# Kernel tuning notes

Measured on AMD Instinct MI355X. Metric: run time of the kernel, lower is better.

Reference implementation:

```python
import jax, jax.numpy as jnp
import numpy as np

HYP_C = 0.1
TAU = 0.1
MRG = 0.1
CLIP_R = 2.3
BS = 1024
NB_PROXIES = 256
SZ_EMBED = 128
T_BATCH = BS * 50
T_LCA = NB_PROXIES * 50


@jax.custom_vjp
def artanh(x):
    xc = jnp.clip(x, -1.0 + 1e-5, 1.0 - 1e-5)
    return 0.5 * (jnp.log1p(xc) - jnp.log1p(-xc))

def _artanh_fwd(x):
    xc = jnp.clip(x, -1.0 + 1e-5, 1.0 - 1e-5)
    return 0.5 * (jnp.log1p(xc) - jnp.log1p(-xc)), xc

def _artanh_bwd(xc, g):
    return (g / (1.0 - xc * xc),)

artanh.defvjp(_artanh_fwd, _artanh_bwd)


@jax.custom_vjp
def riemannian_fix(x):
    # identity fwd; bwd rescales euclidean grad to riemannian grad on the ball
    return x

def _riem_fwd(x):
    return x, x

def _riem_bwd(x, g):
    scale = ((1.0 - HYP_C * jnp.sum(x * x, axis=-1, keepdims=True)) ** 2) / 4.0
    return (g * scale,)

riemannian_fix.defvjp(_riem_fwd, _riem_bwd)


def expmap0(x, c):
    sqrt_c = c ** 0.5
    xn = jnp.maximum(jnp.linalg.norm(x, axis=-1, keepdims=True), 1e-5)
    return jnp.tanh(sqrt_c * xn) * x / (sqrt_c * xn)


def project(x, c):
    norm = jnp.maximum(jnp.linalg.norm(x, axis=-1, keepdims=True), 1e-5)
    maxnorm = (1.0 - 1e-3) / (c ** 0.5)
    return jnp.where(norm > maxnorm, x / norm * maxnorm, x)


def to_poincare(x, c, clip_r):
    xn = jnp.linalg.norm(x, axis=-1, keepdims=True) + 1e-5
    x = x * jnp.minimum(jnp.ones_like(xn), clip_r / xn)
    return riemannian_fix(project(expmap0(x, c), c))


def dist_matrix(x, y, c):
    # ||mobius_add(-x, y)|| computed in closed form (same math as the [N,M,D]
    # num/denom construction in the torch code; num_{nm} = a*( -x_n ) + b*y_m).
    sqrt_c = c ** 0.5
    xy = -jnp.einsum('nd,md->nm', x, y)        # (-x) . y
    x2 = jnp.sum(x * x, axis=-1, keepdims=True)  # [N,1]
    y2t = jnp.sum(y * y, axis=-1)[None, :]       # [1,M]
    a = 1.0 + 2.0 * c * xy + c * y2t             # coeff of -x
    b = 1.0 - c * x2                             # coeff of y
    denom = 1.0 + 2.0 * c * xy + (c ** 2) * x2 * y2t
    num_sq = a * a * x2 + 2.0 * a * b * xy + b * b * y2t
    norm = jnp.sqrt(jnp.maximum(num_sq, 1e-12)) / jnp.abs(denom + 1e-5)
    return (2.0 / sqrt_c) * artanh(sqrt_c * norm)


def gumbel_softmax_hard(logits, g):
    # straight-through hard gumbel softmax (tau=1 as in F.gumbel_softmax default)
    y = jax.nn.softmax(logits + g, axis=-1)
    hard = jax.nn.one_hot(jnp.argmax(y, axis=-1), y.shape[-1], dtype=y.dtype)
    return y + jax.lax.stop_gradient(hard - y)


def compute_ghhc(cp_dist, trip, g):
    i, j, k = trip[0], trip[1], trip[2]
    di, dj, dk = cp_dist[i], cp_dist[j], cp_dist[k]   # [T,P] each
    max_ij = jnp.maximum(di, dj)
    p_ij = gumbel_softmax_hard(-max_ij / TAU, g[0])
    max_ijk = jnp.maximum(dk, max_ij)
    p_ijk = gumbel_softmax_hard(-max_ijk / TAU, g[1])
    diff_lca = (jnp.argmax(p_ij, -1) != jnp.argmax(p_ijk, -1)).astype(cp_dist.dtype)
    d_i_ij = jnp.sum(di * p_ij, axis=1)
    d_i_ijk = jnp.sum(di * p_ijk, axis=1)
    d_j_ij = jnp.sum(dj * p_ij, axis=1)
    d_j_ijk = jnp.sum(dj * p_ijk, axis=1)
    d_k_ij = jnp.sum(dk * p_ij, axis=1)
    d_k_ijk = jnp.sum(dk * p_ijk, axis=1)
    hc = (jax.nn.relu(d_i_ij - d_i_ijk + MRG)
          + jax.nn.relu(d_j_ij - d_j_ijk + MRG)
          + jax.nn.relu(d_k_ijk - d_k_ij + MRG))
    return jnp.mean(hc * diff_lca)


def hp_loss(z_s, t_s, lcas, trip1, trip2, trip3, trip4, g1, g2, g3, g4):
    bs = z_s.shape[0]
    lh = to_poincare(lcas, HYP_C, CLIP_R)
    all_nodes = jnp.concatenate([z_s, lh], axis=0)
    D = dist_matrix(all_nodes, all_nodes, HYP_C)
    t_all = jnp.concatenate([t_s, lh], axis=0)
    Dt = dist_matrix(t_all, t_all, HYP_C)
    loss = compute_ghhc(D[:bs, bs:], trip1, g1)
    loss = loss + compute_ghhc(D[bs:, bs:], trip2, g2)
    loss = loss + compute_ghhc(Dt[:bs, bs:], trip3, g3)
    loss = loss + compute_ghhc(Dt[bs:, bs:], trip4, g4)
    return loss


def setup_inputs() -> dict:
    key = jax.random.key(0)
    ks = jax.random.split(key, 12)
    z_s = jax.random.normal(ks[0], (BS, SZ_EMBED), dtype=jnp.float32)
    t_s = jax.random.normal(ks[1], (BS, SZ_EMBED), dtype=jnp.float32)
    y = jax.random.uniform(ks[2], (BS, 24), dtype=jnp.float32)
    # lcas param init: randn / sqrt(d) * clip_r * 0.9
    lcas = jax.random.normal(ks[3], (NB_PROXIES, SZ_EMBED), dtype=jnp.float32)
    lcas = lcas / np.sqrt(SZ_EMBED) * CLIP_R * 0.9
    trip1 = jax.random.randint(ks[4], (3, T_BATCH), 0, BS, dtype=jnp.int32)
    trip2 = jax.random.randint(ks[5], (3, T_LCA), 0, NB_PROXIES, dtype=jnp.int32)
    trip3 = jax.random.randint(ks[6], (3, T_BATCH), 0, BS, dtype=jnp.int32)
    trip4 = jax.random.randint(ks[7], (3, T_LCA), 0, NB_PROXIES, dtype=jnp.int32)
    g1 = jax.random.gumbel(ks[8], (2, T_BATCH, NB_PROXIES), dtype=jnp.float32)
    g2 = jax.random.gumbel(ks[9], (2, T_LCA, NB_PROXIES), dtype=jnp.float32)
    g3 = jax.random.gumbel(ks[10], (2, T_BATCH, NB_PROXIES), dtype=jnp.float32)
    g4 = jax.random.gumbel(ks[11], (2, T_LCA, NB_PROXIES), dtype=jnp.float32)
    return {"z_s": z_s, "t_s": t_s, "y": y, "lcas": lcas,
            "trip1": trip1, "trip2": trip2, "trip3": trip3, "trip4": trip4,
            "g1": g1, "g2": g2, "g3": g3, "g4": g4}


def reference(z_s, t_s, y, lcas, trip1, trip2, trip3, trip4, g1, g2, g3, g4):
    # y only feeds the detached numpy mining loop in the original; the mined
    # triplets are supplied precomputed (trip1..4), so y does not enter the math.
    return hp_loss(z_s, t_s, lcas, trip1, trip2, trip3, trip4, g1, g2, g3, g4)
```

## Files before the change

kernel.cpp:

```cpp
#include <hip/hip_runtime.h>
#include <cstddef>
#include <stdint.h>

#define HYP_C   0.1f
#define SQRT_C  0.31622776601683794f
#define CLIP_R  2.3f
#define MRG     0.1f
#define NPROX   256
#define DIM     128

#define OFF_LH   0
#define OFF_LHT  32768
#define OFF_LN2  65536
#define OFF_D1   65792
#define OFF_D2   327936
#define OFF_D3   393472

__global__ __launch_bounds__(128)
void to_poincare_kernel(const float* __restrict__ lcas,
                        float* __restrict__ ws,
                        float* __restrict__ out)
{
    const int row = blockIdx.x;
    const int k   = threadIdx.x;
    if (row == 0 && k == 0) out[0] = 0.0f;

    float v  = lcas[row * DIM + k];
    float ss = v * v;
    #pragma unroll
    for (int off = 32; off >= 1; off >>= 1)
        ss += __shfl_xor(ss, off, 64);
    __shared__ float wpart[2];
    if ((k & 63) == 0) wpart[k >> 6] = ss;
    __syncthreads();
    const float sumsq = wpart[0] + wpart[1];

    const float s1 = sqrtf(sumsq);
    const float xn = s1 + 1e-5f;
    const float f1 = fminf(1.0f, CLIP_R / xn);
    const float xn2 = fmaxf(f1 * s1, 1e-5f);
    const float th  = tanhf(SQRT_C * xn2);
    const float f2  = th / (SQRT_C * xn2);
    const float nr      = fmaxf(f2 * f1 * s1, 1e-5f);
    const float maxnorm = (1.0f - 1e-3f) / SQRT_C;
    const float f3      = (nr > maxnorm) ? (maxnorm / nr) : 1.0f;

    const float f  = f3 * f2 * f1;
    const float lv = f * v;
    ws[OFF_LH  + row * DIM + k]   = lv;
    ws[OFF_LHT + k * NPROX + row] = lv;
    if (k == 0) ws[OFF_LN2 + row] = f * f * sumsq;
}

__global__ __launch_bounds__(256)
void dist_all_kernel(const float* __restrict__ z,
                     const float* __restrict__ t,
                     float* __restrict__ ws, int nb1)
{
    const float* lhT = ws + OFF_LHT;
    const float* ln2 = ws + OFF_LN2;

    int b = blockIdx.x;
    const float* X; float* Dout; int row0;
    if (b < nb1)            { X = z;            Dout = ws + OFF_D1; row0 = b * 4; }
    else if (b < nb1 + 64)  { X = ws + OFF_LH;  Dout = ws + OFF_D2; row0 = (b - nb1) * 4; }
    else                    { X = t;            Dout = ws + OFF_D3; row0 = (b - nb1 - 64) * 4; }

    __shared__ float xs[4][DIM];
    __shared__ float sx2[4];

    for (int idx = threadIdx.x; idx < 4 * DIM; idx += 256)
        xs[idx / DIM][idx % DIM] = X[row0 * DIM + idx];
    __syncthreads();

    const int wid  = threadIdx.x >> 6;
    const int lane = threadIdx.x & 63;
    {
        float a = xs[wid][lane];
        float c = xs[wid][lane + 64];
        float s = a * a + c * c;
        #pragma unroll
        for (int off = 32; off >= 1; off >>= 1)
            s += __shfl_xor(s, off, 64);
        if (lane == 0) sx2[wid] = s;
    }
    __syncthreads();

    const int m = threadIdx.x;
    float dot0 = 0.f, dot1 = 0.f, dot2 = 0.f, dot3 = 0.f;
    #pragma unroll 4
    for (int k = 0; k < DIM; ++k) {
        const float lv = lhT[k * NPROX + m];
        dot0 = fmaf(xs[0][k], lv, dot0);
        dot1 = fmaf(xs[1][k], lv, dot1);
        dot2 = fmaf(xs[2][k], lv, dot2);
        dot3 = fmaf(xs[3][k], lv, dot3);
    }

    const float y2 = ln2[m];
    float dots[4] = {dot0, dot1, dot2, dot3};
    #pragma unroll
    for (int r = 0; r < 4; ++r) {
        const float x2 = sx2[r];
        const float xy = -dots[r];
        const float a  = 1.0f + 2.0f * HYP_C * xy + HYP_C * y2;
        const float bb = 1.0f - HYP_C * x2;
        const float denom  = 1.0f + 2.0f * HYP_C * xy + HYP_C * HYP_C * x2 * y2;
        const float num_sq = a * a * x2 + 2.0f * a * bb * xy + bb * bb * y2;
        const float nrm = sqrtf(fmaxf(num_sq, 1e-12f)) / fabsf(denom + 1e-5f);
        float u = SQRT_C * nrm;
        u = fminf(fmaxf(u, -1.0f + 1e-5f), 1.0f - 1e-5f);
        const float d = (2.0f / SQRT_C) * (0.5f * (log1pf(u) - log1pf(-u)));
        Dout[(size_t)(row0 + r) * NPROX + m] = d;
    }
}

__device__ __forceinline__ uint32_t fkey(float f) {
    uint32_t b = __float_as_uint(f);
    return (b & 0x80000000u) ? ~b : (b | 0x80000000u);
}

__device__ __forceinline__ float bcast_col(float4 v, int col) {
    const int comp = col & 3;
    float x = (comp == 0) ? v.x : (comp == 1) ? v.y : (comp == 2) ? v.z : v.w;
    return __shfl(x, col >> 2, 64);
}

__global__ __launch_bounds__(256)
void ghhc_fused_kernel(const float* __restrict__ Da, const float* __restrict__ Db,
                       const float* __restrict__ Dc, const float* __restrict__ Dd,
                       const int* __restrict__ ta, const int* __restrict__ tb,
                       const int* __restrict__ tc, const int* __restrict__ td,
                       const float* __restrict__ ga, const float* __restrict__ gb,
                       const float* __restrict__ gc, const float* __restrict__ gd,
                       int Ta, int Tb, int Tc, int Td,
                       float sa, float sb, float sc_, float sd,
                       float* __restrict__ out)
{
    const int lane = threadIdx.x & 63;
    const int gw   = (blockIdx.x << 2) | (threadIdx.x >> 6);
    const int nw   = gridDim.x << 2;
    const int b1 = Ta, b2 = Ta + Tb, b3 = Ta + Tb + Tc;
    const int P  = (b3 + Td) >> 1;
    float acc = 0.0f;

    for (int p = gw; p < P; p += nw) {
        const int t0 = p << 1;
        const float* D; const int* tr; const float* g; int Tt; float sc; int t;
        if (t0 < b1)      { D = Da; tr = ta; g = ga; Tt = Ta; sc = sa;  t = t0; }
        else if (t0 < b2) { D = Db; tr = tb; g = gb; Tt = Tb; sc = sb;  t = t0 - b1; }
        else if (t0 < b3) { D = Dc; tr = tc; g = gc; Tt = Tc; sc = sc_; t = t0 - b2; }
        else              { D = Dd; tr = td; g = gd; Tt = Td; sc = sd;  t = t0 - b3; }

        const int2 I2 = *(const int2*)(tr + t);
        const int2 J2 = *(const int2*)(tr + Tt + t);
        const int2 K2 = *(const int2*)(tr + 2 * Tt + t);
        const int I[2] = {I2.x, I2.y}, J[2] = {J2.x, J2.y}, Kk[2] = {K2.x, K2.y};

        float4 di[2], dj[2], dk[2];
        unsigned long long KA[2], KB[2];

        #pragma unroll
        for (int u = 0; u < 2; ++u) {
            di[u] = ((const float4*)(D + (size_t)I[u]  * NPROX))[lane];
            dj[u] = ((const float4*)(D + (size_t)J[u]  * NPROX))[lane];
            dk[u] = ((const float4*)(D + (size_t)Kk[u] * NPROX))[lane];
            const float4 G0 = ((const float4*)(g + (size_t)(t + u) * NPROX))[lane];
            const float4 G1 = ((const float4*)(g + ((size_t)Tt + t + u) * NPROX))[lane];

            const float m1x = fmaxf(di[u].x, dj[u].x), m1y = fmaxf(di[u].y, dj[u].y),
                        m1z = fmaxf(di[u].z, dj[u].z), m1w = fmaxf(di[u].w, dj[u].w);
            const int p0 = lane << 2;

            float s0 = (-m1x) / 0.1f + G0.x;
            float s1 = (-m1y) / 0.1f + G0.y;
            float s2 = (-m1z) / 0.1f + G0.z;
            float s3 = (-m1w) / 0.1f + G0.w;
            float bv = s0; int bi = p0;
            if (s1 > bv) { bv = s1; bi = p0 + 1; }
            if (s2 > bv) { bv = s2; bi = p0 + 2; }
            if (s3 > bv) { bv = s3; bi = p0 + 3; }
            KA[u] = ((unsigned long long)fkey(bv) << 32) | (unsigned)(255 - bi);

            const float m2x = fmaxf(dk[u].x, m1x), m2y = fmaxf(dk[u].y, m1y),
                        m2z = fmaxf(dk[u].z, m1z), m2w = fmaxf(dk[u].w, m1w);
            float u0 = (-m2x) / 0.1f + G1.x;
            float u1 = (-m2y) / 0.1f + G1.y;
            float u2 = (-m2z) / 0.1f + G1.z;
            float u3 = (-m2w) / 0.1f + G1.w;
            float cv = u0; int ci = p0;
            if (u1 > cv) { cv = u1; ci = p0 + 1; }
            if (u2 > cv) { cv = u2; ci = p0 + 2; }
            if (u3 > cv) { cv = u3; ci = p0 + 3; }
            KB[u] = ((unsigned long long)fkey(cv) << 32) | (unsigned)(255 - ci);
        }

        #pragma unroll
        for (int off = 1; off < 64; off <<= 1) {
            unsigned long long q;
            q = __shfl_xor(KA[0], off, 64); if (q > KA[0]) KA[0] = q;
            q = __shfl_xor(KB[0], off, 64); if (q > KB[0]) KB[0] = q;
            q = __shfl_xor(KA[1], off, 64); if (q > KA[1]) KA[1] = q;
            q = __shfl_xor(KB[1], off, 64); if (q > KB[1]) KB[1] = q;
        }

        #pragma unroll
        for (int u = 0; u < 2; ++u) {
            const int A = 255 - (int)(KA[u] & 0xFFu);
            const int B = 255 - (int)(KB[u] & 0xFFu);
            if (A != B) {
                const float diA = bcast_col(di[u], A), diB = bcast_col(di[u], B);
                const float djA = bcast_col(dj[u], A), djB = bcast_col(dj[u], B);
                const float dkA = bcast_col(dk[u], A), dkB = bcast_col(dk[u], B);
                const float hc = fmaxf(diA - diB + MRG, 0.0f)
                               + fmaxf(djA - djB + MRG, 0.0f)
                               + fmaxf(dkB - dkA + MRG, 0.0f);
                acc += hc * sc;
            }
        }
    }

    __shared__ float wsum[4];
    if (lane == 0) wsum[threadIdx.x >> 6] = acc;
    __syncthreads();
    if (threadIdx.x == 0)
        atomicAdd(out, wsum[0] + wsum[1] + wsum[2] + wsum[3]);
}

extern "C" void kernel_launch(void* const* d_in, const int* in_sizes, int n_in,
                              void* d_out, int out_size, void* d_ws, size_t ws_size,
                              hipStream_t stream)
{
    const float* z_s  = (const float*)d_in[0];
    const float* t_s  = (const float*)d_in[1];
    const float* lcas = (const float*)d_in[3];
    const int* trip1 = (const int*)d_in[4];
    const int* trip2 = (const int*)d_in[5];
    const int* trip3 = (const int*)d_in[6];
    const int* trip4 = (const int*)d_in[7];
    const float* g1 = (const float*)d_in[8];
    const float* g2 = (const float*)d_in[9];
    const float* g3 = (const float*)d_in[10];
    const float* g4 = (const float*)d_in[11];
    float* out = (float*)d_out;
    float* ws  = (float*)d_ws;

    const int T1 = in_sizes[4] / 3;
    const int T2 = in_sizes[5] / 3;
    const int T3 = in_sizes[6] / 3;
    const int T4 = in_sizes[7] / 3;
    const int BS = in_sizes[0] / DIM;
    const int nb1 = BS / 4;

    to_poincare_kernel<<<NPROX, 128, 0, stream>>>(lcas, ws, out);

    dist_all_kernel<<<2 * nb1 + 64, 256, 0, stream>>>(z_s, t_s, ws, nb1);

    ghhc_fused_kernel<<<4096, 256, 0, stream>>>(
        ws + OFF_D1, ws + OFF_D2, ws + OFF_D3, ws + OFF_D2,
        trip1, trip2, trip3, trip4,
        g1, g2, g3, g4,
        T1, T2, T3, T4,
        1.0f / (float)T1, 1.0f / (float)T2, 1.0f / (float)T3, 1.0f / (float)T4,
        out);
}
```

Measured before the change: 318.9 us.

## Split each wavefront into half-wave triplet lanes with ballot-based argmax

The triplet loss kernel now assigns one triplet to each 32-lane half of a wavefront. Each lane handles 8 columns through a tournament max, and the argmax is found with a half-wave max-shuffle followed by a ballot in place of 64-bit key shuffles. The main loop processes two pairs per iteration for more memory-level parallelism, and the grid is halved to match. The selected distances are re-read from global memory instead of being broadcast by shuffle. The distance kernel's dot-product loop is also changed to read shared memory with float4 loads.

```diff
diff --git a/kernel.cpp b/kernel.cpp
--- a/kernel.cpp
+++ b/kernel.cpp
@@ -88,13 +88,20 @@
 
     const int m = threadIdx.x;
     float dot0 = 0.f, dot1 = 0.f, dot2 = 0.f, dot3 = 0.f;
-    #pragma unroll 4
-    for (int k = 0; k < DIM; ++k) {
-        const float lv = lhT[k * NPROX + m];
-        dot0 = fmaf(xs[0][k], lv, dot0);
-        dot1 = fmaf(xs[1][k], lv, dot1);
-        dot2 = fmaf(xs[2][k], lv, dot2);
-        dot3 = fmaf(xs[3][k], lv, dot3);
+    #pragma unroll 8
+    for (int k = 0; k < DIM; k += 4) {
+        const float4 x0 = *(const float4*)&xs[0][k];
+        const float4 x1 = *(const float4*)&xs[1][k];
+        const float4 x2 = *(const float4*)&xs[2][k];
+        const float4 x3 = *(const float4*)&xs[3][k];
+        const float l0 = lhT[(k + 0) * NPROX + m];
+        const float l1 = lhT[(k + 1) * NPROX + m];
+        const float l2 = lhT[(k + 2) * NPROX + m];
+        const float l3 = lhT[(k + 3) * NPROX + m];
+        dot0 = fmaf(x0.x, l0, fmaf(x0.y, l1, fmaf(x0.z, l2, fmaf(x0.w, l3, dot0))));
+        dot1 = fmaf(x1.x, l0, fmaf(x1.y, l1, fmaf(x1.z, l2, fmaf(x1.w, l3, dot1))));
+        dot2 = fmaf(x2.x, l0, fmaf(x2.y, l1, fmaf(x2.z, l2, fmaf(x2.w, l3, dot2))));
+        dot3 = fmaf(x3.x, l0, fmaf(x3.y, l1, fmaf(x3.z, l2, fmaf(x3.w, l3, dot3))));
     }
 
     const float y2 = ln2[m];
@@ -115,15 +122,97 @@
     }
 }
 
-__device__ __forceinline__ uint32_t fkey(float f) {
-    uint32_t b = __float_as_uint(f);
-    return (b & 0x80000000u) ? ~b : (b | 0x80000000u);
-}
-
-__device__ __forceinline__ float bcast_col(float4 v, int col) {
-    const int comp = col & 3;
-    float x = (comp == 0) ? v.x : (comp == 1) ? v.y : (comp == 2) ? v.z : v.w;
-    return __shfl(x, col >> 2, 64);
+__device__ __forceinline__ void tourn8(const float4 a, const float4 b,
+                                       float& bv, int& bi)
+{
+    float v01 = a.x; int i01 = 0;
+    if (a.y > v01) { v01 = a.y; i01 = 1; }
+    float v23 = a.z; int i23 = 2;
+    if (a.w > v23) { v23 = a.w; i23 = 3; }
+    float v45 = b.x; int i45 = 4;
+    if (b.y > v45) { v45 = b.y; i45 = 5; }
+    float v67 = b.z; int i67 = 6;
+    if (b.w > v67) { v67 = b.w; i67 = 7; }
+    if (v23 > v01) { v01 = v23; i01 = i23; }
+    if (v67 > v45) { v45 = v67; i45 = i67; }
+    bv = v01; bi = i01;
+    if (v45 > bv) { bv = v45; bi = i45; }
+}
+
+__device__ __forceinline__ int half_argmax(float lv, int bi, int base, int half)
+{
+    float hv = lv;
+    #pragma unroll
+    for (int off = 1; off <= 16; off <<= 1)
+        hv = fmaxf(hv, __shfl_xor(hv, off, 64));
+    const unsigned long long m = __ballot(lv == hv);
+    const unsigned int m32 = (unsigned int)(m >> (half << 5));
+    const int owner = (half << 5) + (__ffs(m32) - 1);
+    return __shfl(base + bi, owner, 64);
+}
+
+__device__ __forceinline__ float do_pair(const float* __restrict__ D,
+                                         const int* __restrict__ tr,
+                                         const float* __restrict__ g,
+                                         int Tt, int t, float sc,
+                                         int half, int hl)
+{
+    const int tt = t + half;
+    const int i = tr[tt];
+    const int j = tr[Tt + tt];
+    const int k = tr[2 * Tt + tt];
+
+    const float4* Di = (const float4*)(D + (size_t)i * NPROX);
+    const float4* Dj = (const float4*)(D + (size_t)j * NPROX);
+    const float4* Dk = (const float4*)(D + (size_t)k * NPROX);
+    const float4* G0 = (const float4*)(g + (size_t)tt * NPROX);
+    const float4* G1 = (const float4*)(g + ((size_t)Tt + tt) * NPROX);
+    const int q = hl * 2;
+    const float4 di0 = Di[q], di1 = Di[q + 1];
+    const float4 dj0 = Dj[q], dj1 = Dj[q + 1];
+    const float4 dk0 = Dk[q], dk1 = Dk[q + 1];
+    const float4 g00 = G0[q], g01 = G0[q + 1];
+    const float4 g10 = G1[q], g11 = G1[q + 1];
+
+    float4 m10, m11;
+    m10.x = fmaxf(di0.x, dj0.x); m10.y = fmaxf(di0.y, dj0.y);
+    m10.z = fmaxf(di0.z, dj0.z); m10.w = fmaxf(di0.w, dj0.w);
+    m11.x = fmaxf(di1.x, dj1.x); m11.y = fmaxf(di1.y, dj1.y);
+    m11.z = fmaxf(di1.z, dj1.z); m11.w = fmaxf(di1.w, dj1.w);
+
+    float4 s0, s1;
+    s0.x = fmaf(m10.x, -10.0f, g00.x); s0.y = fmaf(m10.y, -10.0f, g00.y);
+    s0.z = fmaf(m10.z, -10.0f, g00.z); s0.w = fmaf(m10.w, -10.0f, g00.w);
+    s1.x = fmaf(m11.x, -10.0f, g01.x); s1.y = fmaf(m11.y, -10.0f, g01.y);
+    s1.z = fmaf(m11.z, -10.0f, g01.z); s1.w = fmaf(m11.w, -10.0f, g01.w);
+
+    float bv; int bi;
+    tourn8(s0, s1, bv, bi);
+    const int A = half_argmax(bv, bi, hl * 8, half);
+
+    float4 m20, m21;
+    m20.x = fmaxf(dk0.x, m10.x); m20.y = fmaxf(dk0.y, m10.y);
+    m20.z = fmaxf(dk0.z, m10.z); m20.w = fmaxf(dk0.w, m10.w);
+    m21.x = fmaxf(dk1.x, m11.x); m21.y = fmaxf(dk1.y, m11.y);
+    m21.z = fmaxf(dk1.z, m11.z); m21.w = fmaxf(dk1.w, m11.w);
+
+    float4 u0, u1;
+    u0.x = fmaf(m20.x, -10.0f, g10.x); u0.y = fmaf(m20.y, -10.0f, g10.y);
+    u0.z = fmaf(m20.z, -10.0f, g10.z); u0.w = fmaf(m20.w, -10.0f, g10.w);
+    u1.x = fmaf(m21.x, -10.0f, g11.x); u1.y = fmaf(m21.y, -10.0f, g11.y);
+    u1.z = fmaf(m21.z, -10.0f, g11.z); u1.w = fmaf(m21.w, -10.0f, g11.w);
+
+    float cv; int ci;
+    tourn8(u0, u1, cv, ci);
+    const int B = half_argmax(cv, ci, hl * 8, half);
+
+    const float diA = D[(size_t)i * NPROX + A], diB = D[(size_t)i * NPROX + B];
+    const float djA = D[(size_t)j * NPROX + A], djB = D[(size_t)j * NPROX + B];
+    const float dkA = D[(size_t)k * NPROX + A], dkB = D[(size_t)k * NPROX + B];
+    const float hc = fmaxf(diA - diB + MRG, 0.0f)
+                   + fmaxf(djA - djB + MRG, 0.0f)
+                   + fmaxf(dkB - dkA + MRG, 0.0f);
+    return (A != B) ? hc * sc : 0.0f;
 }
 
 __global__ __launch_bounds__(256)
@@ -138,90 +227,43 @@
                        float* __restrict__ out)
 {
     const int lane = threadIdx.x & 63;
+    const int half = lane >> 5;
+    const int hl   = lane & 31;
     const int gw   = (blockIdx.x << 2) | (threadIdx.x >> 6);
     const int nw   = gridDim.x << 2;
     const int b1 = Ta, b2 = Ta + Tb, b3 = Ta + Tb + Tc;
     const int P  = (b3 + Td) >> 1;
     float acc = 0.0f;
 
-    for (int p = gw; p < P; p += nw) {
-        const int t0 = p << 1;
-        const float* D; const int* tr; const float* g; int Tt; float sc; int t;
-        if (t0 < b1)      { D = Da; tr = ta; g = ga; Tt = Ta; sc = sa;  t = t0; }
-        else if (t0 < b2) { D = Db; tr = tb; g = gb; Tt = Tb; sc = sb;  t = t0 - b1; }
-        else if (t0 < b3) { D = Dc; tr = tc; g = gc; Tt = Tc; sc = sc_; t = t0 - b2; }
-        else              { D = Dd; tr = td; g = gd; Tt = Td; sc = sd;  t = t0 - b3; }
-
-        const int2 I2 = *(const int2*)(tr + t);
-        const int2 J2 = *(const int2*)(tr + Tt + t);
-        const int2 K2 = *(const int2*)(tr + 2 * Tt + t);
-        const int I[2] = {I2.x, I2.y}, J[2] = {J2.x, J2.y}, Kk[2] = {K2.x, K2.y};
-
-        float4 di[2], dj[2], dk[2];
-        unsigned long long KA[2], KB[2];
-
-        #pragma unroll
-        for (int u = 0; u < 2; ++u) {
-            di[u] = ((const float4*)(D + (size_t)I[u]  * NPROX))[lane];
-            dj[u] = ((const float4*)(D + (size_t)J[u]  * NPROX))[lane];
-            dk[u] = ((const float4*)(D + (size_t)Kk[u] * NPROX))[lane];
-            const float4 G0 = ((const float4*)(g + (size_t)(t + u) * NPROX))[lane];
-            const float4 G1 = ((const float4*)(g + ((size_t)Tt + t + u) * NPROX))[lane];
-
-            const float m1x = fmaxf(di[u].x, dj[u].x), m1y = fmaxf(di[u].y, dj[u].y),
-                        m1z = fmaxf(di[u].z, dj[u].z), m1w = fmaxf(di[u].w, dj[u].w);
-            const int p0 = lane << 2;
-
-            float s0 = (-m1x) / 0.1f + G0.x;
-            float s1 = (-m1y) / 0.1f + G0.y;
-            float s2 = (-m1z) / 0.1f + G0.z;
-            float s3 = (-m1w) / 0.1f + G0.w;
-            float bv = s0; int bi = p0;
-            if (s1 > bv) { bv = s1; bi = p0 + 1; }
-            if (s2 > bv) { bv = s2; bi = p0 + 2; }
-            if (s3 > bv) { bv = s3; bi = p0 + 3; }
-            KA[u] = ((unsigned long long)fkey(bv) << 32) | (unsigned)(255 - bi);
-
-            const float m2x = fmaxf(dk[u].x, m1x), m2y = fmaxf(dk[u].y, m1y),
-                        m2z = fmaxf(dk[u].z, m1z), m2w = fmaxf(dk[u].w, m1w);
-            float u0 = (-m2x) / 0.1f + G1.x;
-            float u1 = (-m2y) / 0.1f + G1.y;
-            float u2 = (-m2z) / 0.1f + G1.z;
-            float u3 = (-m2w) / 0.1f + G1.w;
-            float cv = u0; int ci = p0;
-            if (u1 > cv) { cv = u1; ci = p0 + 1; }
-            if (u2 > cv) { cv = u2; ci = p0 + 2; }
-            if (u3 > cv) { cv = u3; ci = p0 + 3; }
-            KB[u] = ((unsigned long long)fkey(cv) << 32) | (unsigned)(255 - ci);
+    for (int p = gw; p < P; p += 2 * nw) {
+        {
+            const int t0 = p << 1;
+            const float* D; const int* tr; const float* g; int Tt; float sc; int t;
+            if (t0 < b1)      { D = Da; tr = ta; g = ga; Tt = Ta; sc = sa;  t = t0; }
+            else if (t0 < b2) { D = Db; tr = tb; g = gb; Tt = Tb; sc = sb;  t = t0 - b1; }
+            else if (t0 < b3) { D = Dc; tr = tc; g = gc; Tt = Tc; sc = sc_; t = t0 - b2; }
+            else              { D = Dd; tr = td; g = gd; Tt = Td; sc = sd;  t = t0 - b3; }
+            acc += do_pair(D, tr, g, Tt, t, sc, half, hl);
         }
-
-        #pragma unroll
-        for (int off = 1; off < 64; off <<= 1) {
-            unsigned long long q;
-            q = __shfl_xor(KA[0], off, 64); if (q > KA[0]) KA[0] = q;
-            q = __shfl_xor(KB[0], off, 64); if (q > KB[0]) KB[0] = q;
-            q = __shfl_xor(KA[1], off, 64); if (q > KA[1]) KA[1] = q;
-            q = __shfl_xor(KB[1], off, 64); if (q > KB[1]) KB[1] = q;
-        }
-
-        #pragma unroll
-        for (int u = 0; u < 2; ++u) {
-            const int A = 255 - (int)(KA[u] & 0xFFu);
-            const int B = 255 - (int)(KB[u] & 0xFFu);
-            if (A != B) {
-                const float diA = bcast_col(di[u], A), diB = bcast_col(di[u], B);
-                const float djA = bcast_col(dj[u], A), djB = bcast_col(dj[u], B);
-                const float dkA = bcast_col(dk[u], A), dkB = bcast_col(dk[u], B);
-                const float hc = fmaxf(diA - diB + MRG, 0.0f)
-                               + fmaxf(djA - djB + MRG, 0.0f)
-                               + fmaxf(dkB - dkA + MRG, 0.0f);
-                acc += hc * sc;
-            }
+        {
+            const int p2v = p + nw;
+            const bool ok = p2v < P;
+            const int p2 = ok ? p2v : p;
+            const int t0 = p2 << 1;
+            const float* D; const int* tr; const float* g; int Tt; float sc; int t;
+            if (t0 < b1)      { D = Da; tr = ta; g = ga; Tt = Ta; sc = sa;  t = t0; }
+            else if (t0 < b2) { D = Db; tr = tb; g = gb; Tt = Tb; sc = sb;  t = t0 - b1; }
+            else if (t0 < b3) { D = Dc; tr = tc; g = gc; Tt = Tc; sc = sc_; t = t0 - b2; }
+            else              { D = Dd; tr = td; g = gd; Tt = Td; sc = sd;  t = t0 - b3; }
+            const float v = do_pair(D, tr, g, Tt, t, sc, half, hl);
+            acc += ok ? v : 0.0f;
         }
     }
 
+    const float other = __shfl_xor(acc, 32, 64);
+    const float tot = acc + other;
     __shared__ float wsum[4];
-    if (lane == 0) wsum[threadIdx.x >> 6] = acc;
+    if (lane == 0) wsum[threadIdx.x >> 6] = tot;
     __syncthreads();
     if (threadIdx.x == 0)
         atomicAdd(out, wsum[0] + wsum[1] + wsum[2] + wsum[3]);
@@ -256,7 +298,7 @@
 
     dist_all_kernel<<<2 * nb1 + 64, 256, 0, stream>>>(z_s, t_s, ws, nb1);
 
-    ghhc_fused_kernel<<<4096, 256, 0, stream>>>(
+    ghhc_fused_kernel<<<2048, 256, 0, stream>>>(
         ws + OFF_D1, ws + OFF_D2, ws + OFF_D3, ws + OFF_D2,
         trip1, trip2, trip3, trip4,
         g1, g2, g3, g4,
```

Measured after the change: 301.0 us. -5.6%, faster.

## Map each triplet to a 16-lane group with DPP argmax reductions

Applied to the files above, without the earlier changes.

The fused triplet-loss kernel drops the one-wavefront-per-pair grid-stride loop with 64-bit shuffle argmax. Each 64-thread block now takes 32 triplets from one segment, with four 16-lane groups each handling one triplet. The groups use a value-then-index argmax built on DPP row reductions and re-read the two selected columns directly from global memory. This cuts cross-lane shuffle traffic and branchy segment dispatch, but launches many more small blocks and issues one atomic per block. The distance kernel's inner loop is also reworked to read the shared x rows as float4 with deeper unrolling.

```diff
diff --git a/kernel.cpp b/kernel.cpp
--- a/kernel.cpp
+++ b/kernel.cpp
@@ -88,13 +88,20 @@
 
     const int m = threadIdx.x;
     float dot0 = 0.f, dot1 = 0.f, dot2 = 0.f, dot3 = 0.f;
-    #pragma unroll 4
-    for (int k = 0; k < DIM; ++k) {
-        const float lv = lhT[k * NPROX + m];
-        dot0 = fmaf(xs[0][k], lv, dot0);
-        dot1 = fmaf(xs[1][k], lv, dot1);
-        dot2 = fmaf(xs[2][k], lv, dot2);
-        dot3 = fmaf(xs[3][k], lv, dot3);
+    #pragma unroll 8
+    for (int k = 0; k < DIM; k += 4) {
+        const float4 x0 = *(const float4*)&xs[0][k];
+        const float4 x1 = *(const float4*)&xs[1][k];
+        const float4 x2 = *(const float4*)&xs[2][k];
+        const float4 x3 = *(const float4*)&xs[3][k];
+        const float l0 = lhT[(k + 0) * NPROX + m];
+        const float l1 = lhT[(k + 1) * NPROX + m];
+        const float l2 = lhT[(k + 2) * NPROX + m];
+        const float l3 = lhT[(k + 3) * NPROX + m];
+        dot0 = fmaf(x0.x, l0, fmaf(x0.y, l1, fmaf(x0.z, l2, fmaf(x0.w, l3, dot0))));
+        dot1 = fmaf(x1.x, l0, fmaf(x1.y, l1, fmaf(x1.z, l2, fmaf(x1.w, l3, dot1))));
+        dot2 = fmaf(x2.x, l0, fmaf(x2.y, l1, fmaf(x2.z, l2, fmaf(x2.w, l3, dot2))));
+        dot3 = fmaf(x3.x, l0, fmaf(x3.y, l1, fmaf(x3.z, l2, fmaf(x3.w, l3, dot3))));
     }
 
     const float y2 = ln2[m];
@@ -115,18 +122,38 @@
     }
 }
 
-__device__ __forceinline__ uint32_t fkey(float f) {
-    uint32_t b = __float_as_uint(f);
-    return (b & 0x80000000u) ? ~b : (b | 0x80000000u);
-}
-
-__device__ __forceinline__ float bcast_col(float4 v, int col) {
-    const int comp = col & 3;
-    float x = (comp == 0) ? v.x : (comp == 1) ? v.y : (comp == 2) ? v.z : v.w;
-    return __shfl(x, col >> 2, 64);
-}
-
-__global__ __launch_bounds__(256)
+__device__ __forceinline__ float dpp_fmax16(float x) {
+    int o;
+    o = __builtin_amdgcn_update_dpp(0, __float_as_int(x), 0x121, 0xF, 0xF, true);
+    x = fmaxf(x, __int_as_float(o));
+    o = __builtin_amdgcn_update_dpp(0, __float_as_int(x), 0x122, 0xF, 0xF, true);
+    x = fmaxf(x, __int_as_float(o));
+    o = __builtin_amdgcn_update_dpp(0, __float_as_int(x), 0x124, 0xF, 0xF, true);
+    x = fmaxf(x, __int_as_float(o));
+    o = __builtin_amdgcn_update_dpp(0, __float_as_int(x), 0x128, 0xF, 0xF, true);
+    x = fmaxf(x, __int_as_float(o));
+    return x;
+}
+
+__device__ __forceinline__ int dpp_imax16(int x) {
+    int o;
+    o = __builtin_amdgcn_update_dpp(0, x, 0x121, 0xF, 0xF, true); x = max(x, o);
+    o = __builtin_amdgcn_update_dpp(0, x, 0x122, 0xF, 0xF, true); x = max(x, o);
+    o = __builtin_amdgcn_update_dpp(0, x, 0x124, 0xF, 0xF, true); x = max(x, o);
+    o = __builtin_amdgcn_update_dpp(0, x, 0x128, 0xF, 0xF, true); x = max(x, o);
+    return x;
+}
+
+__device__ __forceinline__ void amax4(float v0, float v1, float v2, float v3,
+                                      int base, float& lv, int& li)
+{
+    if (v0 > lv) { lv = v0; li = base; }
+    if (v1 > lv) { lv = v1; li = base + 1; }
+    if (v2 > lv) { lv = v2; li = base + 2; }
+    if (v3 > lv) { lv = v3; li = base + 3; }
+}
+
+__global__ __launch_bounds__(64, 4)
 void ghhc_fused_kernel(const float* __restrict__ Da, const float* __restrict__ Db,
                        const float* __restrict__ Dc, const float* __restrict__ Dd,
                        const int* __restrict__ ta, const int* __restrict__ tb,
@@ -135,96 +162,78 @@
                        const float* __restrict__ gc, const float* __restrict__ gd,
                        int Ta, int Tb, int Tc, int Td,
                        float sa, float sb, float sc_, float sd,
+                       int nba, int nbb, int nbc,
                        float* __restrict__ out)
 {
-    const int lane = threadIdx.x & 63;
-    const int gw   = (blockIdx.x << 2) | (threadIdx.x >> 6);
-    const int nw   = gridDim.x << 2;
-    const int b1 = Ta, b2 = Ta + Tb, b3 = Ta + Tb + Tc;
-    const int P  = (b3 + Td) >> 1;
+    const int lane = threadIdx.x;
+    const int grp  = lane >> 4;
+    const int hl   = lane & 15;
+
+    const int b = blockIdx.x;
+    const float* D; const int* tr; const float* g; int Tt; float sc; int lb;
+    if (b < nba)                   { D = Da; tr = ta; g = ga; Tt = Ta; sc = sa;  lb = b; }
+    else if (b < nba + nbb)        { D = Db; tr = tb; g = gb; Tt = Tb; sc = sb;  lb = b - nba; }
+    else if (b < nba + nbb + nbc)  { D = Dc; tr = tc; g = gc; Tt = Tc; sc = sc_; lb = b - nba - nbb; }
+    else                           { D = Dd; tr = td; g = gd; Tt = Td; sc = sd;  lb = b - nba - nbb - nbc; }
+
+    const int tstart = lb * 32;
     float acc = 0.0f;
 
-    for (int p = gw; p < P; p += nw) {
-        const int t0 = p << 1;
-        const float* D; const int* tr; const float* g; int Tt; float sc; int t;
-        if (t0 < b1)      { D = Da; tr = ta; g = ga; Tt = Ta; sc = sa;  t = t0; }
-        else if (t0 < b2) { D = Db; tr = tb; g = gb; Tt = Tb; sc = sb;  t = t0 - b1; }
-        else if (t0 < b3) { D = Dc; tr = tc; g = gc; Tt = Tc; sc = sc_; t = t0 - b2; }
-        else              { D = Dd; tr = td; g = gd; Tt = Td; sc = sd;  t = t0 - b3; }
-
-        const int2 I2 = *(const int2*)(tr + t);
-        const int2 J2 = *(const int2*)(tr + Tt + t);
-        const int2 K2 = *(const int2*)(tr + 2 * Tt + t);
-        const int I[2] = {I2.x, I2.y}, J[2] = {J2.x, J2.y}, Kk[2] = {K2.x, K2.y};
-
-        float4 di[2], dj[2], dk[2];
-        unsigned long long KA[2], KB[2];
+    #pragma unroll 2
+    for (int it = 0; it < 8; ++it) {
+        const int tt = tstart + it * 4 + grp;
+        const bool ok = tt < Tt;
+        const int ts = ok ? tt : (Tt - 1);
+        const int i = tr[ts], j = tr[Tt + ts], kk = tr[2 * Tt + ts];
+
+        const float4* Di = (const float4*)(D + (size_t)i  * NPROX);
+        const float4* Dj = (const float4*)(D + (size_t)j  * NPROX);
+        const float4* Dk = (const float4*)(D + (size_t)kk * NPROX);
+        const float4* G0 = (const float4*)(g + (size_t)ts * NPROX);
+        const float4* G1 = (const float4*)(g + ((size_t)Tt + ts) * NPROX);
+
+        float lvA = -__builtin_inff(), lvB = -__builtin_inff();
+        int   liA = 0, liB = 0;
 
         #pragma unroll
-        for (int u = 0; u < 2; ++u) {
-            di[u] = ((const float4*)(D + (size_t)I[u]  * NPROX))[lane];
-            dj[u] = ((const float4*)(D + (size_t)J[u]  * NPROX))[lane];
-            dk[u] = ((const float4*)(D + (size_t)Kk[u] * NPROX))[lane];
-            const float4 G0 = ((const float4*)(g + (size_t)(t + u) * NPROX))[lane];
-            const float4 G1 = ((const float4*)(g + ((size_t)Tt + t + u) * NPROX))[lane];
-
-            const float m1x = fmaxf(di[u].x, dj[u].x), m1y = fmaxf(di[u].y, dj[u].y),
-                        m1z = fmaxf(di[u].z, dj[u].z), m1w = fmaxf(di[u].w, dj[u].w);
-            const int p0 = lane << 2;
-
-            float s0 = (-m1x) / 0.1f + G0.x;
-            float s1 = (-m1y) / 0.1f + G0.y;
-            float s2 = (-m1z) / 0.1f + G0.z;
-            float s3 = (-m1w) / 0.1f + G0.w;
-            float bv = s0; int bi = p0;
-            if (s1 > bv) { bv = s1; bi = p0 + 1; }
-            if (s2 > bv) { bv = s2; bi = p0 + 2; }
-            if (s3 > bv) { bv = s3; bi = p0 + 3; }
-            KA[u] = ((unsigned long long)fkey(bv) << 32) | (unsigned)(255 - bi);
-
-            const float m2x = fmaxf(dk[u].x, m1x), m2y = fmaxf(dk[u].y, m1y),
-                        m2z = fmaxf(dk[u].z, m1z), m2w = fmaxf(dk[u].w, m1w);
-            float u0 = (-m2x) / 0.1f + G1.x;
-            float u1 = (-m2y) / 0.1f + G1.y;
-            float u2 = (-m2z) / 0.1f + G1.z;
-            float u3 = (-m2w) / 0.1f + G1.w;
-            float cv = u0; int ci = p0;
-            if (u1 > cv) { cv = u1; ci = p0 + 1; }
-            if (u2 > cv) { cv = u2; ci = p0 + 2; }
-            if (u3 > cv) { cv = u3; ci = p0 + 3; }
-            KB[u] = ((unsigned long long)fkey(cv) << 32) | (unsigned)(255 - ci);
+        for (int m = 0; m < 4; ++m) {
+            const int q = m * 16 + hl;
+            const float4 di = Di[q], dj = Dj[q], dk = Dk[q];
+            const float4 g0 = G0[q], g1 = G1[q];
+
+            const float m1x = fmaxf(di.x, dj.x), m1y = fmaxf(di.y, dj.y),
+                        m1z = fmaxf(di.z, dj.z), m1w = fmaxf(di.w, dj.w);
+            const float sx = fmaf(m1x, -10.0f, g0.x), sy = fmaf(m1y, -10.0f, g0.y),
+                        sz = fmaf(m1z, -10.0f, g0.z), sw = fmaf(m1w, -10.0f, g0.w);
+            const float m2x = fmaxf(dk.x, m1x), m2y = fmaxf(dk.y, m1y),
+                        m2z = fmaxf(dk.z, m1z), m2w = fmaxf(dk.w, m1w);
+            const float ux = fmaf(m2x, -10.0f, g1.x), uy = fmaf(m2y, -10.0f, g1.y),
+                        uz = fmaf(m2z, -10.0f, g1.z), uw = fmaf(m2w, -10.0f, g1.w);
+
+            const int base = m * 64 + hl * 4;
+            amax4(sx, sy, sz, sw, base, lvA, liA);
+            amax4(ux, uy, uz, uw, base, lvB, liB);
         }
 
-        #pragma unroll
-        for (int off = 1; off < 64; off <<= 1) {
-            unsigned long long q;
-            q = __shfl_xor(KA[0], off, 64); if (q > KA[0]) KA[0] = q;
-            q = __shfl_xor(KB[0], off, 64); if (q > KB[0]) KB[0] = q;
-            q = __shfl_xor(KA[1], off, 64); if (q > KA[1]) KA[1] = q;
-            q = __shfl_xor(KB[1], off, 64); if (q > KB[1]) KB[1] = q;
-        }
-
-        #pragma unroll
-        for (int u = 0; u < 2; ++u) {
-            const int A = 255 - (int)(KA[u] & 0xFFu);
-            const int B = 255 - (int)(KB[u] & 0xFFu);
-            if (A != B) {
-                const float diA = bcast_col(di[u], A), diB = bcast_col(di[u], B);
-                const float djA = bcast_col(dj[u], A), djB = bcast_col(dj[u], B);
-                const float dkA = bcast_col(dk[u], A), dkB = bcast_col(dk[u], B);
-                const float hc = fmaxf(diA - diB + MRG, 0.0f)
-                               + fmaxf(djA - djB + MRG, 0.0f)
-                               + fmaxf(dkB - dkA + MRG, 0.0f);
-                acc += hc * sc;
-            }
-        }
-    }
-
-    __shared__ float wsum[4];
-    if (lane == 0) wsum[threadIdx.x >> 6] = acc;
-    __syncthreads();
-    if (threadIdx.x == 0)
-        atomicAdd(out, wsum[0] + wsum[1] + wsum[2] + wsum[3]);
+        const float gvA = dpp_fmax16(lvA);
+        const int   A   = 255 - dpp_imax16((lvA == gvA) ? (255 - liA) : 0);
+        const float gvB = dpp_fmax16(lvB);
+        const int   B   = 255 - dpp_imax16((lvB == gvB) ? (255 - liB) : 0);
+
+        const float diA = D[(size_t)i  * NPROX + A], diB = D[(size_t)i  * NPROX + B];
+        const float djA = D[(size_t)j  * NPROX + A], djB = D[(size_t)j  * NPROX + B];
+        const float dkA = D[(size_t)kk * NPROX + A], dkB = D[(size_t)kk * NPROX + B];
+        const float hc = fmaxf(diA - diB + MRG, 0.0f)
+                       + fmaxf(djA - djB + MRG, 0.0f)
+                       + fmaxf(dkB - dkA + MRG, 0.0f);
+        acc += (ok && (A != B) && (hl == 0)) ? hc * sc : 0.0f;
+    }
+
+    #pragma unroll
+    for (int off = 32; off >= 1; off >>= 1)
+        acc += __shfl_xor(acc, off, 64);
+    if (lane == 0)
+        atomicAdd(out, acc);
 }
 
 extern "C" void kernel_launch(void* const* d_in, const int* in_sizes, int n_in,
@@ -256,11 +265,16 @@
 
     dist_all_kernel<<<2 * nb1 + 64, 256, 0, stream>>>(z_s, t_s, ws, nb1);
 
-    ghhc_fused_kernel<<<4096, 256, 0, stream>>>(
+    const int nbA = (T1 + 31) / 32;
+    const int nbB = (T2 + 31) / 32;
+    const int nbC = (T3 + 31) / 32;
+    const int nbD = (T4 + 31) / 32;
+    ghhc_fused_kernel<<<nbA + nbB + nbC + nbD, 64, 0, stream>>>(
         ws + OFF_D1, ws + OFF_D2, ws + OFF_D3, ws + OFF_D2,
         trip1, trip2, trip3, trip4,
         g1, g2, g3, g4,
         T1, T2, T3, T4,
         1.0f / (float)T1, 1.0f / (float)T2, 1.0f / (float)T3, 1.0f / (float)T4,
+        nbA, nbB, nbC,
         out);
 }
```

New measurement: 350.9 us. 10.0% more time.
